# Kernel optimization log

Hardware: AMD Instinct MI355X
Metric: run time of the kernel (lower is better)

Reference implementation:

```python
import jax, jax.numpy as jnp
import numpy as np

DIST_POWER = 1  # distance_power from init

def setup_inputs() -> dict:
    key = jax.random.key(0)
    k1, k2 = jax.random.split(key)
    N, D, C = 8192, 128, 256
    l_embeds = jax.random.normal(k1, (N, D), dtype=jnp.float32)
    l_labels = jax.random.randint(k2, (N,), 0, C, dtype=jnp.int64)
    return {"l_embeds": l_embeds, "l_labels": l_labels}

def reference(l_embeds, l_labels):
    # normalize_embeds=True
    x = l_embeds / jnp.linalg.norm(l_embeds, axis=1, keepdims=True)
    sq = jnp.sum(x * x, axis=1)  # [N]
    d2 = sq[:, None] + sq[None, :] - 2.0 * jnp.matmul(x, x.T)
    dist = jnp.sqrt(jnp.maximum(d2, 0.0))  # distance_power == 1
    if DIST_POWER != 1:
        dist = dist ** DIST_POWER
    N = x.shape[0]
    same = l_labels[:, None] == l_labels[None, :]
    eye = jnp.eye(N, dtype=bool)
    pos_mask = same & ~eye          # positives, diagonal removed (l is r)
    neg_mask = ~same
    # pos_dist = distmat * pos_mask (nan -> 0); hardest positive = argmax
    pos_dist = jnp.where(pos_mask, dist, 0.0)
    hardest_pos_inds = jnp.argmax(pos_dist, axis=1)
    # neg_dist = distmat with same-label entries set to +inf; hardest negative = argmin
    neg_dist = jnp.where(neg_mask, dist, jnp.inf)
    hardest_neg_inds = jnp.argmin(neg_dist, axis=1)
    anchor_inds = jnp.arange(N)
    # keep mask (all True by construction of labels); returned instead of
    # data-dependent boolean filtering to stay jit-compatible
    keep = jnp.any(pos_mask, axis=1) & jnp.any(neg_mask, axis=1)
    return anchor_inds, hardest_pos_inds, hardest_neg_inds, keep
```

## Files before the change

### kernel.cpp

```cpp
#include <hip/hip_runtime.h>
#include <math.h>

#define N 8192
#define D 128
#define NT 64
#define NBLK (NT * (NT + 1) / 2)

typedef __attribute__((ext_vector_type(8))) short bf8;
typedef __attribute__((ext_vector_type(4))) float f4;

__device__ __forceinline__ unsigned short bf16_rtne(float f) {
    unsigned u = __float_as_uint(f);
    u += 0x7FFF + ((u >> 16) & 1);
    return (unsigned short)(u >> 16);
}
__device__ __forceinline__ float bf16_tof(unsigned short h) {
    return __uint_as_float((unsigned)h << 16);
}

__device__ __forceinline__ void async_cp16(const void* g, void* l) {
    __builtin_amdgcn_global_load_lds(
        (const __attribute__((address_space(1))) unsigned*)g,
        (__attribute__((address_space(3))) unsigned*)l, 16, 0, 0);
}

__global__ __launch_bounds__(256) void prep_kernel(
    const float* __restrict__ x, short* __restrict__ H,
    float* __restrict__ sq,
    unsigned long long* __restrict__ pos_pack,
    unsigned long long* __restrict__ neg_pack) {
    __shared__ float Xs[32 * 129];
    const int t = threadIdx.x;
    const int r0 = blockIdx.x * 32;

    if (t < 32) { pos_pack[r0 + t] = 0ULL; neg_pack[r0 + t] = ~0ULL; }

#pragma unroll
    for (int p = 0; p < 4; ++p) {
        const int lin = p * 256 + t;
        const int row = lin >> 5;
        const int c0 = (lin & 31) << 2;
        const float4 v = *(const float4*)(x + (size_t)(r0 + row) * D + c0);
        float* dst = &Xs[row * 129 + c0];
        dst[0] = v.x; dst[1] = v.y; dst[2] = v.z; dst[3] = v.w;
    }
    __syncthreads();

    const int r = t >> 3, q8 = t & 7;
    float* src = &Xs[r * 129 + q8 * 16];
    float s = 0.f;
#pragma unroll
    for (int i = 0; i < 16; ++i) s = fmaf(src[i], src[i], s);
    s += __shfl_xor(s, 1, 64);
    s += __shfl_xor(s, 2, 64);
    s += __shfl_xor(s, 4, 64);
    const float nrm = sqrtf(s);
    float t2 = 0.f;
#pragma unroll
    for (int i = 0; i < 16; ++i) {
        const float n = src[i] / nrm;
        src[i] = n;
        t2 = fmaf(n, n, t2);
    }
    t2 += __shfl_xor(t2, 1, 64);
    t2 += __shfl_xor(t2, 2, 64);
    t2 += __shfl_xor(t2, 4, 64);
    if (q8 == 0) sq[r0 + r] = t2;

    const size_t gbase = (size_t)(r0 + r) * D + q8 * 16;
#pragma unroll
    for (int g = 0; g < 4; ++g) {
        short4 o1, o2, o3;
        short* p1 = (short*)&o1; short* p2 = (short*)&o2; short* p3 = (short*)&o3;
#pragma unroll
        for (int i = 0; i < 4; ++i) {
            const float n = src[g * 4 + i];
            const unsigned short h1 = bf16_rtne(n);
            const float r1 = n - bf16_tof(h1);
            const unsigned short h2 = bf16_rtne(r1);
            const float r2 = r1 - bf16_tof(h2);
            const unsigned short h3 = bf16_rtne(r2);
            p1[i] = (short)h1; p2[i] = (short)h2; p3[i] = (short)h3;
        }
        *(short4*)(H + gbase + g * 4)                     = o1;
        *(short4*)(H + (size_t)N * D + gbase + g * 4)     = o2;
        *(short4*)(H + (size_t)2 * N * D + gbase + g * 4) = o3;
    }
}

__device__ __forceinline__ unsigned int fbits(float f) {
    union { float f; unsigned int u; } x; x.f = f; return x.u;
}
__device__ __forceinline__ unsigned long long pack_pos(float v, int j) {
    return ((unsigned long long)fbits(v) << 32) | (unsigned int)(8191 - j);
}
__device__ __forceinline__ unsigned long long pack_neg(float v, int j) {
    return ((unsigned long long)fbits(v) << 32) | (unsigned int)j;
}
__device__ __forceinline__ void red_max(float& v, int& j, int mask) {
    const float ov = __shfl_xor(v, mask, 64);
    const int   oj = __shfl_xor(j, mask, 64);
    if (ov > v || (ov == v && oj < j)) { v = ov; j = oj; }
}
__device__ __forceinline__ void red_min(float& v, int& j, int mask) {
    const float ov = __shfl_xor(v, mask, 64);
    const int   oj = __shfl_xor(j, mask, 64);
    if (ov < v || (ov == v && oj < j)) { v = ov; j = oj; }
}

__global__ __launch_bounds__(256, 3) void miner_kernel(
    const short* __restrict__ H, const float* __restrict__ sq,
    const int* __restrict__ labels,
    unsigned long long* __restrict__ pos_pack,
    unsigned long long* __restrict__ neg_pack) {
    __shared__ __align__(16) short sB[2 * 12288];
    __shared__ float sqS[256];
    __shared__ int   lbS[256];

    const int t = threadIdx.x;
    const int w = t >> 6;
    const int l = t & 63;
    const int quad = l >> 4;
    const int l16 = l & 15;

    const int b = blockIdx.x;
    int bi = (int)((129.0f - sqrtf(16641.0f - 8.0f * (float)b)) * 0.5f);
    while (bi > 0 && (bi * NT - bi * (bi - 1) / 2) > b) --bi;
    while (((bi + 1) * NT - (bi + 1) * bi / 2) <= b) ++bi;
    const int bj = bi + (b - (bi * NT - bi * (bi - 1) / 2));
    const int I0 = bi * 128, J0 = bj * 128;
    const bool diag = (bi == bj);

    float psq; int plb;
    {
        const int idx = ((t < 128) ? I0 : J0) + (t & 127);
        psq = sq[idx]; plb = labels[idx];
    }

    int gOffB[6], lOffB[6];
#pragma unroll
    for (int p = 0; p < 6; ++p) {
        const int limb = p >> 1;
        const int c2   = (p & 1) * 256 + t;
        const int smp  = c2 >> 2;
        const int sub  = c2 & 3;
        gOffB[p] = limb * (N * D) + (J0 + smp) * D + sub * 8;
        lOffB[p] = (limb * 128 + smp) * 32 + sub * 8;
    }
    int aGoff[3];
#pragma unroll
    for (int la = 0; la < 3; ++la)
        aGoff[la] = la * (N * D) + (I0 + w * 32 + l16) * D + quad * 8;

    f4 acc[2][8];
#pragma unroll
    for (int rt = 0; rt < 2; ++rt)
#pragma unroll
        for (int ct = 0; ct < 8; ++ct) acc[rt][ct] = (f4){0.f, 0.f, 0.f, 0.f};

    bf8 aF[2][3][2];
#pragma unroll
    for (int p = 0; p < 6; ++p)
        async_cp16(H + (size_t)gOffB[p], sB + lOffB[p]);
#pragma unroll
    for (int la = 0; la < 3; ++la)
#pragma unroll
        for (int rt = 0; rt < 2; ++rt)
            aF[0][la][rt] = *(const bf8*)(H + (size_t)(aGoff[la] + rt * 2048));

#pragma unroll
    for (int q = 0; q < 4; ++q) {
        const int cur = q & 1, nxt = cur ^ 1;
        const short* sBc = sB + cur * 12288;

        if (q < 3) {
            short* sBn = sB + nxt * 12288;
            const int kn = (q + 1) * 32;
#pragma unroll
            for (int p = 0; p < 6; ++p)
                async_cp16(H + (size_t)(gOffB[p] + kn), sBn + lOffB[p]);
#pragma unroll
            for (int la = 0; la < 3; ++la)
#pragma unroll
                for (int rt = 0; rt < 2; ++rt)
                    aF[nxt][la][rt] = *(const bf8*)
                        (H + (size_t)(aGoff[la] + rt * 2048 + kn));
            asm volatile("s_waitcnt vmcnt(12)" ::: "memory");
        } else {
            asm volatile("s_waitcnt vmcnt(0)" ::: "memory");
        }
        __builtin_amdgcn_s_barrier();
        __builtin_amdgcn_sched_barrier(0);

        __builtin_amdgcn_s_setprio(1);
#pragma unroll
        for (int ct = 0; ct < 8; ++ct) {
            bf8 bF[3];
#pragma unroll
            for (int lb = 0; lb < 3; ++lb)
                bF[lb] = *(const bf8*)
                    &sBc[(lb * 128 + ct * 16 + l16) * 32 + quad * 8];
#pragma unroll
            for (int rt = 0; rt < 2; ++rt) {
                acc[rt][ct] = __builtin_amdgcn_mfma_f32_16x16x32_bf16(
                    aF[cur][0][rt], bF[0], acc[rt][ct], 0, 0, 0);
                acc[rt][ct] = __builtin_amdgcn_mfma_f32_16x16x32_bf16(
                    aF[cur][0][rt], bF[1], acc[rt][ct], 0, 0, 0);
                acc[rt][ct] = __builtin_amdgcn_mfma_f32_16x16x32_bf16(
                    aF[cur][0][rt], bF[2], acc[rt][ct], 0, 0, 0);
                acc[rt][ct] = __builtin_amdgcn_mfma_f32_16x16x32_bf16(
                    aF[cur][1][rt], bF[0], acc[rt][ct], 0, 0, 0);
                acc[rt][ct] = __builtin_amdgcn_mfma_f32_16x16x32_bf16(
                    aF[cur][1][rt], bF[1], acc[rt][ct], 0, 0, 0);
                acc[rt][ct] = __builtin_amdgcn_mfma_f32_16x16x32_bf16(
                    aF[cur][2][rt], bF[0], acc[rt][ct], 0, 0, 0);
            }
        }
        __builtin_amdgcn_s_setprio(0);

        if (q < 2) {
            asm volatile("" ::: "memory");
            __builtin_amdgcn_s_barrier();
            __builtin_amdgcn_sched_barrier(0);
        }
    }

    sqS[t] = psq; lbS[t] = plb;
    __syncthreads();
    const float* sqI = sqS;       const float* sqJ = sqS + 128;
    const int*   lbI = lbS;       const int*   lbJ = lbS + 128;

    int ljv[8];
#pragma unroll
    for (int ct = 0; ct < 8; ++ct) ljv[ct] = lbJ[ct * 16 + l16];

    {
        float sjv[8];
#pragma unroll
        for (int ct = 0; ct < 8; ++ct) sjv[ct] = sqJ[ct * 16 + l16];
#pragma unroll
        for (int rt = 0; rt < 2; ++rt)
#pragma unroll
            for (int r = 0; r < 4; ++r) {
                const float si = sqI[w * 32 + rt * 16 + quad * 4 + r];
#pragma unroll
                for (int ct = 0; ct < 8; ++ct)
                    acc[rt][ct][r] =
                        fmaxf(si + sjv[ct] - 2.0f * acc[rt][ct][r], 0.0f);
            }
    }

#pragma unroll
    for (int rt = 0; rt < 2; ++rt)
#pragma unroll
        for (int r = 0; r < 4; ++r) {
            const int lr = w * 32 + rt * 16 + quad * 4 + r;
            const int grow = I0 + lr;
            const int liv = lbI[lr];
            float bpv = -1.0f, bnv = INFINITY; int bpj = 0, bnj = 0;
            if (diag) {
#pragma unroll
                for (int ct = 0; ct < 8; ++ct) {
                    const float d2 = acc[rt][ct][r];
                    const int col = J0 + ct * 16 + l16;
                    const bool same = (liv == ljv[ct]);
                    const float vp = (same && grow != col) ? d2 : 0.0f;
                    if (vp > bpv) { bpv = vp; bpj = col; }
                    const float vn = same ? INFINITY : d2;
                    if (vn < bnv) { bnv = vn; bnj = col; }
                }
            } else {
#pragma unroll
                for (int ct = 0; ct < 8; ++ct) {
                    const float d2 = acc[rt][ct][r];
                    const int col = J0 + ct * 16 + l16;
                    const bool same = (liv == ljv[ct]);
                    const float vp = same ? d2 : 0.0f;
                    if (vp > bpv) { bpv = vp; bpj = col; }
                    const float vn = same ? INFINITY : d2;
                    if (vn < bnv) { bnv = vn; bnj = col; }
                }
            }
            red_max(bpv, bpj, 1); red_max(bpv, bpj, 2);
            red_max(bpv, bpj, 4); red_max(bpv, bpj, 8);
            red_min(bnv, bnj, 1); red_min(bnv, bnj, 2);
            red_min(bnv, bnj, 4); red_min(bnv, bnj, 8);
            if (l16 == 0) {
                atomicMax(&pos_pack[grow], pack_pos(bpv, bpj));
                atomicMin(&neg_pack[grow], pack_neg(bnv, bnj));
            }
        }

    if (!diag) {
        unsigned long long* scr = (unsigned long long*)sB;
#pragma unroll
        for (int ct = 0; ct < 8; ++ct) {
            float bpv = -1.0f, bnv = INFINITY; int bpj = 0, bnj = 0;
#pragma unroll
            for (int rt = 0; rt < 2; ++rt)
#pragma unroll
                for (int r = 0; r < 4; ++r) {
                    const int lr = w * 32 + rt * 16 + quad * 4 + r;
                    const float d2 = acc[rt][ct][r];
                    const int row = I0 + lr;
                    const bool same = (lbI[lr] == ljv[ct]);
                    const float vp = same ? d2 : 0.0f;
                    if (vp > bpv) { bpv = vp; bpj = row; }
                    const float vn = same ? INFINITY : d2;
                    if (vn < bnv) { bnv = vn; bnj = row; }
                }
            red_max(bpv, bpj, 16); red_min(bnv, bnj, 16);
            red_max(bpv, bpj, 32); red_min(bnv, bnj, 32);
            if (quad == 0) {
                scr[w * 128 + ct * 16 + l16]       = pack_pos(bpv, bpj);
                scr[512 + w * 128 + ct * 16 + l16] = pack_neg(bnv, bnj);
            }
        }
        __syncthreads();
        if (t < 128) {
            unsigned long long mp = 0ULL, mn = ~0ULL;
#pragma unroll
            for (int ww = 0; ww < 4; ++ww) {
                const unsigned long long p = scr[ww * 128 + t];
                const unsigned long long qq = scr[512 + ww * 128 + t];
                if (p > mp) mp = p;
                if (qq < mn) mn = qq;
            }
            atomicMax(&pos_pack[J0 + t], mp);
            atomicMin(&neg_pack[J0 + t], mn);
        }
    }
}

__global__ void finalize_kernel(const unsigned long long* __restrict__ pos_pack,
                                const unsigned long long* __restrict__ neg_pack,
                                int* __restrict__ out) {
    const int r = blockIdx.x * 256 + threadIdx.x;
    const unsigned long long pp = pos_pack[r];
    const unsigned long long np = neg_pack[r];
    out[r]         = r;
    out[N + r]     = 8191 - (int)(pp & 0xFFFFFFFFULL);
    out[2 * N + r] = (int)(np & 0xFFFFFFFFULL);
    out[3 * N + r] = (pp != 0ULL && np != ~0ULL) ? 1 : 0;
}

extern "C" void kernel_launch(void* const* d_in, const int* in_sizes, int n_in,
                              void* d_out, int out_size, void* d_ws, size_t ws_size,
                              hipStream_t stream) {
    const float* x      = (const float*)d_in[0];
    const int*   labels = (const int*)d_in[1];
    int* out = (int*)d_out;

    short* H = (short*)d_ws;
    float* sq = (float*)(H + (size_t)3 * N * D);
    unsigned long long* pos_pack =
        (unsigned long long*)(sq + N);
    unsigned long long* neg_pack = pos_pack + N;

    prep_kernel<<<N / 32, 256, 0, stream>>>(x, H, sq, pos_pack, neg_pack);
    miner_kernel<<<NBLK, 256, 0, stream>>>(H, sq, labels, pos_pack, neg_pack);
    finalize_kernel<<<N / 256, 256, 0, stream>>>(pos_pack, neg_pack, out);
}
```

Measured before the change: 145.4 us.

## Mine hardest positives per class bucket instead of in the full distance matrix

```diff
diff --git a/kernel.cpp b/kernel.cpp
--- a/kernel.cpp
+++ b/kernel.cpp
@@ -3,6 +3,8 @@
 
 #define N 8192
 #define D 128
+#define C 256
+#define CCAP 96
 #define NT 64
 #define NBLK (NT * (NT + 1) / 2)
 
@@ -24,11 +26,32 @@
         (__attribute__((address_space(3))) unsigned*)l, 16, 0, 0);
 }
 
+__device__ __forceinline__ unsigned int fbits(float f) {
+    union { float f; unsigned int u; } x; x.f = f; return x.u;
+}
+__device__ __forceinline__ unsigned long long pack_pos(float v, int j) {
+    return ((unsigned long long)fbits(v) << 32) | (unsigned int)(8191 - j);
+}
+__device__ __forceinline__ unsigned long long pack_neg(float v, int j) {
+    return ((unsigned long long)fbits(v) << 32) | (unsigned int)j;
+}
+__device__ __forceinline__ void red_max(float& v, int& j, int mask) {
+    const float ov = __shfl_xor(v, mask, 64);
+    const int   oj = __shfl_xor(j, mask, 64);
+    if (ov > v || (ov == v && oj < j)) { v = ov; j = oj; }
+}
+__device__ __forceinline__ void red_min(float& v, int& j, int mask) {
+    const float ov = __shfl_xor(v, mask, 64);
+    const int   oj = __shfl_xor(j, mask, 64);
+    if (ov < v || (ov == v && oj < j)) { v = ov; j = oj; }
+}
+
 __global__ __launch_bounds__(256) void prep_kernel(
-    const float* __restrict__ x, short* __restrict__ H,
-    float* __restrict__ sq,
+    const float* __restrict__ x, const int* __restrict__ labels,
+    short* __restrict__ H, float* __restrict__ sq,
     unsigned long long* __restrict__ pos_pack,
-    unsigned long long* __restrict__ neg_pack) {
+    unsigned long long* __restrict__ neg_pack,
+    int* __restrict__ cnt, int* __restrict__ lists) {
     __shared__ float Xs[32 * 129];
     const int t = threadIdx.x;
     const int r0 = blockIdx.x * 32;
@@ -65,7 +88,12 @@
     t2 += __shfl_xor(t2, 1, 64);
     t2 += __shfl_xor(t2, 2, 64);
     t2 += __shfl_xor(t2, 4, 64);
-    if (q8 == 0) sq[r0 + r] = t2;
+    if (q8 == 0) {
+        sq[r0 + r] = t2;
+        const int lb = labels[r0 + r];
+        const int slot = atomicAdd(&cnt[lb], 1);
+        if (slot < CCAP) lists[lb * CCAP + slot] = r0 + r;
+    }
 
     const size_t gbase = (size_t)(r0 + r) * D + q8 * 16;
 #pragma unroll
@@ -88,30 +116,65 @@
     }
 }
 
-__device__ __forceinline__ unsigned int fbits(float f) {
-    union { float f; unsigned int u; } x; x.f = f; return x.u;
-}
-__device__ __forceinline__ unsigned long long pack_pos(float v, int j) {
-    return ((unsigned long long)fbits(v) << 32) | (unsigned int)(8191 - j);
-}
-__device__ __forceinline__ unsigned long long pack_neg(float v, int j) {
-    return ((unsigned long long)fbits(v) << 32) | (unsigned int)j;
-}
-__device__ __forceinline__ void red_max(float& v, int& j, int mask) {
-    const float ov = __shfl_xor(v, mask, 64);
-    const int   oj = __shfl_xor(j, mask, 64);
-    if (ov > v || (ov == v && oj < j)) { v = ov; j = oj; }
-}
-__device__ __forceinline__ void red_min(float& v, int& j, int mask) {
-    const float ov = __shfl_xor(v, mask, 64);
-    const int   oj = __shfl_xor(j, mask, 64);
-    if (ov < v || (ov == v && oj < j)) { v = ov; j = oj; }
+__global__ __launch_bounds__(256) void posclass_kernel(
+    const short* __restrict__ H, const float* __restrict__ sq,
+    const int* __restrict__ cnt, const int* __restrict__ lists,
+    unsigned long long* __restrict__ pos_pack) {
+    __shared__ float Xc[CCAP * 160];
+    __shared__ float SqS[CCAP];
+    __shared__ int   RwS[CCAP];
+    const int c = blockIdx.x, t = threadIdx.x;
+    const int n = min(cnt[c], CCAP);
+    const int k8 = t & 7;
+    const int g  = t >> 3;
+
+    for (int i = g; i < n; i += 32) {
+        const int row = lists[c * CCAP + i];
+        if (k8 == 0) { SqS[i] = sq[row]; RwS[i] = row; }
+        const int d0 = k8 * 16;
+        const short* h0 = H + (size_t)row * D + d0;
+#pragma unroll
+        for (int d = 0; d < 16; ++d) {
+            const float v = bf16_tof((unsigned short)h0[d])
+                          + bf16_tof((unsigned short)h0[(size_t)N * D + d])
+                          + bf16_tof((unsigned short)h0[(size_t)2 * N * D + d]);
+            Xc[i * 160 + k8 * 20 + d] = v;
+        }
+    }
+    __syncthreads();
+
+    for (int i = g; i < n; i += 32) {
+        float xi[16];
+#pragma unroll
+        for (int d = 0; d < 16; ++d) xi[d] = Xc[i * 160 + k8 * 20 + d];
+        const float si = SqS[i];
+        float best = -1.0f; int bestj = 0x7FFFFFFF;
+        for (int j = 0; j < n; ++j) {
+            if (j == i) continue;
+            const float* xj = &Xc[j * 160 + k8 * 20];
+            float p0 = 0.f, p1 = 0.f;
+#pragma unroll
+            for (int d = 0; d < 16; d += 2) {
+                p0 = fmaf(xi[d],     xj[d],     p0);
+                p1 = fmaf(xi[d + 1], xj[d + 1], p1);
+            }
+            float dot = p0 + p1;
+            dot += __shfl_xor(dot, 1, 64);
+            dot += __shfl_xor(dot, 2, 64);
+            dot += __shfl_xor(dot, 4, 64);
+            const float d2 = fmaxf(si + SqS[j] - 2.0f * dot, 0.0f);
+            const int rj = RwS[j];
+            if (d2 > best || (d2 == best && rj < bestj)) { best = d2; bestj = rj; }
+        }
+        if (k8 == 0)
+            pos_pack[RwS[i]] = (best > 0.0f) ? pack_pos(best, bestj)
+                                             : pack_pos(0.0f, 0);
+    }
 }
 
 __global__ __launch_bounds__(256, 3) void miner_kernel(
     const short* __restrict__ H, const float* __restrict__ sq,
     const int* __restrict__ labels,
-    unsigned long long* __restrict__ pos_pack,
     unsigned long long* __restrict__ neg_pack) {
     __shared__ __align__(16) short sB[2 * 12288];
     __shared__ float sqS[256];
@@ -255,78 +318,46 @@
 #pragma unroll
         for (int r = 0; r < 4; ++r) {
             const int lr = w * 32 + rt * 16 + quad * 4 + r;
-            const int grow = I0 + lr;
             const int liv = lbI[lr];
-            float bpv = -1.0f, bnv = INFINITY; int bpj = 0, bnj = 0;
-            if (diag) {
-#pragma unroll
-                for (int ct = 0; ct < 8; ++ct) {
-                    const float d2 = acc[rt][ct][r];
-                    const int col = J0 + ct * 16 + l16;
-                    const bool same = (liv == ljv[ct]);
-                    const float vp = (same && grow != col) ? d2 : 0.0f;
-                    if (vp > bpv) { bpv = vp; bpj = col; }
-                    const float vn = same ? INFINITY : d2;
-                    if (vn < bnv) { bnv = vn; bnj = col; }
-                }
-            } else {
-#pragma unroll
-                for (int ct = 0; ct < 8; ++ct) {
-                    const float d2 = acc[rt][ct][r];
-                    const int col = J0 + ct * 16 + l16;
-                    const bool same = (liv == ljv[ct]);
-                    const float vp = same ? d2 : 0.0f;
-                    if (vp > bpv) { bpv = vp; bpj = col; }
-                    const float vn = same ? INFINITY : d2;
-                    if (vn < bnv) { bnv = vn; bnj = col; }
-                }
-            }
-            red_max(bpv, bpj, 1); red_max(bpv, bpj, 2);
-            red_max(bpv, bpj, 4); red_max(bpv, bpj, 8);
+            float bnv = INFINITY; int bnj = 0;
+#pragma unroll
+            for (int ct = 0; ct < 8; ++ct) {
+                const float vn = (liv == ljv[ct]) ? INFINITY : acc[rt][ct][r];
+                const int col = J0 + ct * 16 + l16;
+                if (vn < bnv) { bnv = vn; bnj = col; }
+            }
             red_min(bnv, bnj, 1); red_min(bnv, bnj, 2);
             red_min(bnv, bnj, 4); red_min(bnv, bnj, 8);
-            if (l16 == 0) {
-                atomicMax(&pos_pack[grow], pack_pos(bpv, bpj));
-                atomicMin(&neg_pack[grow], pack_neg(bnv, bnj));
-            }
+            if (l16 == 0)
+                atomicMin(&neg_pack[I0 + lr], pack_neg(bnv, bnj));
         }
 
     if (!diag) {
         unsigned long long* scr = (unsigned long long*)sB;
 #pragma unroll
         for (int ct = 0; ct < 8; ++ct) {
-            float bpv = -1.0f, bnv = INFINITY; int bpj = 0, bnj = 0;
+            float bnv = INFINITY; int bnj = 0;
+            const int lj = ljv[ct];
 #pragma unroll
             for (int rt = 0; rt < 2; ++rt)
 #pragma unroll
                 for (int r = 0; r < 4; ++r) {
                     const int lr = w * 32 + rt * 16 + quad * 4 + r;
-                    const float d2 = acc[rt][ct][r];
-                    const int row = I0 + lr;
-                    const bool same = (lbI[lr] == ljv[ct]);
-                    const float vp = same ? d2 : 0.0f;
-                    if (vp > bpv) { bpv = vp; bpj = row; }
-                    const float vn = same ? INFINITY : d2;
-                    if (vn < bnv) { bnv = vn; bnj = row; }
+                    const float vn = (lbI[lr] == lj) ? INFINITY : acc[rt][ct][r];
+                    if (vn < bnv) { bnv = vn; bnj = I0 + lr; }
                 }
-            red_max(bpv, bpj, 16); red_min(bnv, bnj, 16);
-            red_max(bpv, bpj, 32); red_min(bnv, bnj, 32);
-            if (quad == 0) {
-                scr[w * 128 + ct * 16 + l16]       = pack_pos(bpv, bpj);
-                scr[512 + w * 128 + ct * 16 + l16] = pack_neg(bnv, bnj);
-            }
+            red_min(bnv, bnj, 16); red_min(bnv, bnj, 32);
+            if (quad == 0)
+                scr[w * 128 + ct * 16 + l16] = pack_neg(bnv, bnj);
         }
         __syncthreads();
         if (t < 128) {
-            unsigned long long mp = 0ULL, mn = ~0ULL;
+            unsigned long long mn = ~0ULL;
 #pragma unroll
             for (int ww = 0; ww < 4; ++ww) {
-                const unsigned long long p = scr[ww * 128 + t];
-                const unsigned long long qq = scr[512 + ww * 128 + t];
-                if (p > mp) mp = p;
+                const unsigned long long qq = scr[ww * 128 + t];
                 if (qq < mn) mn = qq;
             }
-            atomicMax(&pos_pack[J0 + t], mp);
             atomicMin(&neg_pack[J0 + t], mn);
         }
     }
@@ -356,8 +387,13 @@
     unsigned long long* pos_pack =
         (unsigned long long*)(sq + N);
     unsigned long long* neg_pack = pos_pack + N;
-
-    prep_kernel<<<N / 32, 256, 0, stream>>>(x, H, sq, pos_pack, neg_pack);
-    miner_kernel<<<NBLK, 256, 0, stream>>>(H, sq, labels, pos_pack, neg_pack);
+    int* cnt   = (int*)(neg_pack + N);
+    int* lists = cnt + C;
+
+    hipMemsetAsync(cnt, 0, C * sizeof(int), stream);
+    prep_kernel<<<N / 32, 256, 0, stream>>>(x, labels, H, sq, pos_pack,
+                                            neg_pack, cnt, lists);
+    posclass_kernel<<<C, 256, 0, stream>>>(H, sq, cnt, lists, pos_pack);
+    miner_kernel<<<NBLK, 256, 0, stream>>>(H, sq, labels, neg_pack);
     finalize_kernel<<<N / 256, 256, 0, stream>>>(pos_pack, neg_pack, out);
 }
```

After: 162.6 us. 11.8% more time.
